# Kernel optimization log

Hardware: AMD Instinct MI355X
Metric: run time of the kernel (lower is better)

## Reference

```python
import jax, jax.numpy as jnp
import numpy as np

B, T, C = 2, 2048, 1024
H = 16
D = C // H          # 64
HID = C // 4        # meta_net bottleneck = 256
FF = 4 * C          # 4096


def setup_inputs() -> dict:
    key = jax.random.key(0)
    ks = jax.random.split(key, 11)
    s = lambda fan_in: 1.0 / np.sqrt(fan_in)
    inp = {
        "x": jax.random.normal(ks[0], (B, T, C), jnp.float32),
        # torch nn.Linear weights are [out, in]
        "Wq": jax.random.uniform(ks[1], (C, C), jnp.float32, -s(C), s(C)),
        "Wk": jax.random.uniform(ks[2], (C, C), jnp.float32, -s(C), s(C)),
        "Wv": jax.random.uniform(ks[3], (C, C), jnp.float32, -s(C), s(C)),
        "Wm1": jax.random.uniform(ks[4], (HID, C), jnp.float32, -s(C), s(C)),
        "bm1": jax.random.uniform(ks[5], (HID,), jnp.float32, -s(C), s(C)),
        "Wm2": jax.random.uniform(ks[6], (H, HID), jnp.float32, -s(HID), s(HID)),
        "bm2": jax.random.uniform(ks[7], (H,), jnp.float32, -s(HID), s(HID)),
        "Wproj": jax.random.uniform(ks[8], (C, C), jnp.float32, -s(C), s(C)),
        "Wfc": jax.random.uniform(ks[9], (FF, C), jnp.float32, -s(C), s(C)),
        "Wcp": jax.random.uniform(ks[10], (C, FF), jnp.float32, -s(FF), s(FF)),
    }
    return inp


def _rms_norm(x):
    eps = jnp.finfo(x.dtype).eps
    return x * jax.lax.rsqrt(jnp.mean(jnp.square(x), axis=-1, keepdims=True) + eps)


def reference(x, Wq, Wk, Wv, Wm1, bm1, Wm2, bm2, Wproj, Wfc, Wcp):
    b, t, c = x.shape
    h = Wm2.shape[0]
    d = c // h
    q = (x @ Wq.T).reshape(b, t, h, d)
    k = (x @ Wk.T).reshape(b, t, h, d)
    v = (x @ Wv.T).reshape(b, t, h, d)
    surprise = jax.nn.sigmoid(jnp.maximum(x @ Wm1.T + bm1, 0.0) @ Wm2.T + bm2)  # [b,t,h]
    decay = 1.0 - surprise

    # time-major for scan: [t, b, h, ...]
    qT = jnp.transpose(q, (1, 0, 2, 3))
    kT = jnp.transpose(k, (1, 0, 2, 3))
    vT = jnp.transpose(v, (1, 0, 2, 3))
    dT = jnp.transpose(decay, (1, 0, 2))     # [t,b,h]
    gT = jnp.transpose(surprise, (1, 0, 2))  # [t,b,h]

    def step(state, inp):
        qt, kt, vt, dt, gt = inp
        # state: [b,h,d,d]; decay-gated rank-1 update
        state = state * dt[..., None, None] + gt[..., None, None] * (kt[..., :, None] * vt[..., None, :])
        yt = jnp.einsum('bhd,bhde->bhe', qt, state)
        return state, yt

    state0 = jnp.zeros((b, h, d, d), x.dtype)
    _, ys = jax.lax.scan(step, state0, (qT, kT, vT, dT, gT))  # ys: [t,b,h,d]
    y = jnp.transpose(ys, (1, 0, 2, 3)).reshape(b, t, c)
    y = y @ Wproj.T
    yn = _rms_norm(y)
    mlp = jnp.square(jnp.maximum(yn @ Wfc.T, 0.0)) @ Wcp.T
    return y + mlp
```

## Files before the change

kernel.cpp:

```cpp
#include <hip/hip_runtime.h>
#include <math.h>

#define BB   2
#define TT   2048
#define CC   1024
#define HH   16
#define DD   64
#define HID  256
#define FFD  4096
#define NTOK (BB*TT)
#define CT   64
#define NC   (TT/CT)
#define NBH  (BB*HH)
#define NCHK (NBH*NC)
#define MB   (1048576ULL)

typedef unsigned short u16;
typedef unsigned int   u32;
typedef __attribute__((ext_vector_type(8))) short frag8;
typedef __attribute__((ext_vector_type(4))) float f32x4;

__device__ __forceinline__ float bf2f(u16 h){
    union { u32 u; float f; } c; c.u = ((u32)h) << 16; return c.f;
}
__device__ __forceinline__ u16 f2bf(float f){
    union { float f; u32 u; } c; c.f = f;
    u32 u = c.u;
    u += 0x7FFFu + ((u >> 16) & 1u);
    return (u16)(u >> 16);
}
__device__ __forceinline__ bool is_f32(const u32* flags, int idx) {
    if (idx == -2) return true;
    if (idx < 0)  return false;
    return flags[idx] != 0;
}

__device__ __forceinline__ void gload16(const void* g, void* l) {
    __builtin_amdgcn_global_load_lds(
        (const __attribute__((address_space(1))) u32*)g,
        (__attribute__((address_space(3))) u32*)l, 16, 0, 0);
}

template<int N> __device__ __forceinline__ void wait_vm() {
    if constexpr (N == 0)      asm volatile("s_waitcnt vmcnt(0)" ::: "memory");
    else if constexpr (N == 4) asm volatile("s_waitcnt vmcnt(4)" ::: "memory");
    else                       asm volatile("s_waitcnt vmcnt(6)" ::: "memory");
}
__device__ __forceinline__ void barrier_raw() {
    asm volatile("s_barrier" ::: "memory");
}

struct InPtrs { const void* p[11]; int n[11]; };

__global__ __launch_bounds__(64)
void sniff_kernel(InPtrs ip, u32* __restrict__ flags)
{
    int lane = threadIdx.x;
    u32 f0 = 0;
    for (int i = 0; i < 11; i++) {
        const u16* p = (const u16*)ip.p[i];
        int cap = ip.n[i] < 256 ? ip.n[i] : 256;
        bool ok = true;
        for (int j = lane; j < cap; j += 64) {
            u16 u = p[j];
            u32 e = (u >> 7) & 0xFFu;
            bool good = (u == 0u) || (u == 0x8000u) || (e >= 64u && e < 192u);
            ok = ok && good;
        }
        unsigned long long ball = __ballot(ok);
        u32 fl = (ball == ~0ull) ? 0u : 1u;
        if (ip.n[i] < 64) fl = f0;
        if (i == 0) f0 = fl;
        if (lane == 0) flags[i] = fl;
    }
}

struct ConvArgs {
    const void* src[6];
    u16* dst[6];
    int flag[6];
    int bstart[7];
    int nseg;
};

__global__ __launch_bounds__(256)
void conv_kernel(ConvArgs a, const u32* __restrict__ flags)
{
    int b = blockIdx.x;
    int s = 0;
    #pragma unroll
    for (int i = 1; i < 6; i++) if (i < a.nseg && b >= a.bstart[i]) s = i;
    size_t off = ((size_t)(b - a.bstart[s])) * 2048 + (size_t)threadIdx.x * 8;
    u16* d = a.dst[s] + off;
    if (flags[a.flag[s]] != 0) {
        const float* sp = (const float*)a.src[s] + off;
        float4 x0 = *(const float4*)sp;
        float4 x1 = *(const float4*)(sp + 4);
        u16 buf[8];
        buf[0]=f2bf(x0.x); buf[1]=f2bf(x0.y); buf[2]=f2bf(x0.z); buf[3]=f2bf(x0.w);
        buf[4]=f2bf(x1.x); buf[5]=f2bf(x1.y); buf[6]=f2bf(x1.z); buf[7]=f2bf(x1.w);
        *(uint4*)d = *(uint4*)buf;
    } else {
        *(uint4*)d = *(const uint4*)((const u16*)a.src[s] + off);
    }
}

__device__ __forceinline__ void xcd_map(int i, int NB, int gx, int& bm, int& bn)
{
    int per = NB >> 3;
    int iq  = (i & 7) * per + (i >> 3);
    bm = iq / gx;
    bn = iq % gx;
}

template<int MODE, int BM, int BN, int KS>
__global__ __launch_bounds__(256)
void gemm_nt(const u16* __restrict__ A, const u16* __restrict__ B,
             void* Cm, void* Cm2, const void* aux,
             int M, int N, int K, int lda, int ldb,
             const u32* __restrict__ flags, int oi)
{
    constexpr int MFR = BM / 32;
    constexpr int NFR = BN / 32;
    constexpr int BKE = KS * 32;
    const bool of32 = is_f32(flags, oi);
    __shared__ u16 As[2][KS][BM * 32];
    __shared__ u16 Bs[2][KS][BN * 32];
    const int tid = threadIdx.x;
    int bm, bn;
    xcd_map(blockIdx.x, gridDim.x, N / BN, bm, bn);
    const int z = blockIdx.y;
    const size_t koff = (size_t)z * K;

    const int wave = tid >> 6, lane = tid & 63;
    const int lm = lane & 15, quad = lane >> 4;
    const int wm = (wave >> 1) * (BM / 2), wn = (wave & 1) * (BN / 2);

    const int srow = lane >> 2;
    const int scol = (lane & 3) * 8;
    const int arow = (BM == 128) ? (wave*32 + srow) : (wave*16 + srow);
    const int brow = (BN == 128) ? (wave*32 + srow) : (wave*16 + srow);
    const u16* gA = A + (size_t)(bm*BM + arow)*lda + koff + scol;
    const u16* gB = B + (size_t)(bn*BN + brow)*ldb + koff + scol;
    const size_t a16 = (size_t)16 * lda, b16 = (size_t)16 * ldb;

    f32x4 acc[MFR][NFR];
    #pragma unroll
    for (int i = 0; i < MFR; i++)
        #pragma unroll
        for (int j = 0; j < NFR; j++)
            acc[i][j] = (f32x4){0.f, 0.f, 0.f, 0.f};

    auto stage = [&](int buf, int kk) {
        #pragma unroll
        for (int ks = 0; ks < KS; ks++) {
            if constexpr (BM == 128) {
                gload16(gA + kk + ks*32,       &As[buf][ks][wave*1024]);
                gload16(gA + kk + ks*32 + a16, &As[buf][ks][wave*1024 + 512]);
            } else {
                gload16(gA + kk + ks*32, &As[buf][ks][wave*512]);
            }
            if constexpr (BN == 128) {
                gload16(gB + kk + ks*32,       &Bs[buf][ks][wave*1024]);
                gload16(gB + kk + ks*32 + b16, &Bs[buf][ks][wave*1024 + 512]);
            } else {
                gload16(gB + kk + ks*32, &Bs[buf][ks][wave*512]);
            }
        }
    };

    stage(0, 0);
    __syncthreads();
    int cur = 0;
    for (int k0 = 0; k0 < K; k0 += BKE) {
        if (k0 + BKE < K) stage(cur ^ 1, k0 + BKE);
        #pragma unroll
        for (int ks = 0; ks < KS; ks++) {
            frag8 af[MFR], bfr[NFR];
            #pragma unroll
            for (int i = 0; i < MFR; i++)
                af[i]  = *(frag8*)&As[cur][ks][(wm + i*16 + lm)*32 + quad*8];
            #pragma unroll
            for (int j = 0; j < NFR; j++)
                bfr[j] = *(frag8*)&Bs[cur][ks][(wn + j*16 + lm)*32 + quad*8];
            #pragma unroll
            for (int i = 0; i < MFR; i++)
                #pragma unroll
                for (int j = 0; j < NFR; j++)
                    acc[i][j] = __builtin_amdgcn_mfma_f32_16x16x32_bf16(
                        af[i], bfr[j], acc[i][j], 0, 0, 0);
        }
        __syncthreads();
        cur ^= 1;
    }

    float* outF = (float*)(z ? Cm2 : Cm);
    #pragma unroll
    for (int i = 0; i < MFR; i++) {
        #pragma unroll
        for (int j = 0; j < NFR; j++) {
            const int gcol = bn*BN + wn + j*16 + lm;
            #pragma unroll
            for (int r = 0; r < 4; r++) {
                const int grow = bm*BM + wm + i*16 + quad*4 + r;
                size_t off = (size_t)grow * N + gcol;
                float vv = acc[i][j][r];
                if constexpr (MODE == 0) {
                    outF[off] = vv;
                } else if constexpr (MODE == 2) {
                    vv = fmaxf(vv, 0.f);
                    ((u16*)Cm)[off] = f2bf(vv * vv);
                } else {
                    float res = of32 ? ((const float*)aux)[off]
                                     : bf2f(((const u16*)aux)[off]);
                    vv += res;
                    if (of32) ((float*)Cm)[off] = vv;
                    else      ((u16*)Cm)[off]   = f2bf(vv);
                }
            }
        }
    }
}

__global__ __launch_bounds__(512)
void gemm_fc8(const u16* __restrict__ A, const u16* __restrict__ B,
              u16* __restrict__ C)
{
    __shared__ u16 As[2][256 * 64];
    __shared__ u16 Bs[2][256 * 64];
    const int tid = threadIdx.x;
    int bm, bn;
    xcd_map(blockIdx.x, 256, 16, bm, bn);

    const int w = tid >> 6, lane = tid & 63;
    const int lm = lane & 15, quad = lane >> 4;
    const int wm = (w >> 2) * 128, wn = (w & 3) * 64;

    const int srow = tid >> 3;
    const int scol = (((tid & 7) ^ ((tid >> 3) & 7))) * 8;
    const u16* gA = A + (size_t)(bm*256 + srow)*1024 + scol;
    const u16* gB = B + (size_t)(bn*256 + srow)*1024 + scol;

    auto stageA = [&](int buf, int h, int t1) {
        size_t ko = (size_t)t1 * 64;
        #pragma unroll
        for (int q = 0; q < 2; q++)
            gload16(gA + (size_t)(h*128 + q*64)*1024 + ko,
                    &As[buf][(h*128 + q*64 + w*8)*64]);
    };
    auto stageB = [&](int buf, int h, int t1) {
        size_t ko = (size_t)t1 * 64;
        #pragma unroll
        for (int q = 0; q < 2; q++)
            gload16(gB + (size_t)(h*128 + q*64)*1024 + ko,
                    &Bs[buf][(h*128 + q*64 + w*8)*64]);
    };

    f32x4 acc[8][4];
    #pragma unroll
    for (int i = 0; i < 8; i++)
        #pragma unroll
        for (int j = 0; j < 4; j++)
            acc[i][j] = (f32x4){0.f, 0.f, 0.f, 0.f};

    constexpr int NT = 16;
    stageA(0, 0, 0); stageB(0, 0, 0); stageA(0, 1, 0); stageB(0, 1, 0);

    const int rsw = (lm & 7);
    for (int t = 0; t < NT; ++t) {
        const int cur = t & 1;
        const bool more = (t + 1 < NT);
        #pragma unroll
        for (int p = 0; p < 4; ++p) {
            if (more) {
                if (p == 0)      stageA(cur ^ 1, 0, t + 1);
                else if (p == 1) stageB(cur ^ 1, 0, t + 1);
                else if (p == 2) stageA(cur ^ 1, 1, t + 1);
                else             stageB(cur ^ 1, 1, t + 1);
            }
            if (p == 0) { if (more) wait_vm<6>(); else wait_vm<4>(); }
            if (p == 1) { if (more) wait_vm<4>(); else wait_vm<0>(); }
            barrier_raw();
            const int rh = p >> 1, ch = p & 1;
            frag8 af[4][2], bfr[2][2];
            #pragma unroll
            for (int i = 0; i < 4; i++)
                #pragma unroll
                for (int kk = 0; kk < 2; kk++)
                    af[i][kk] = *(frag8*)&As[cur][(wm + rh*64 + i*16 + lm)*64
                                      + (((kk*4 + quad) ^ rsw) * 8)];
            #pragma unroll
            for (int j = 0; j < 2; j++)
                #pragma unroll
                for (int kk = 0; kk < 2; kk++)
                    bfr[j][kk] = *(frag8*)&Bs[cur][(wn + ch*32 + j*16 + lm)*64
                                      + (((kk*4 + quad) ^ rsw) * 8)];
            __builtin_amdgcn_s_setprio(1);
            #pragma unroll
            for (int kk = 0; kk < 2; kk++)
                #pragma unroll
                for (int i = 0; i < 4; i++)
                    #pragma unroll
                    for (int j = 0; j < 2; j++)
                        acc[rh*4 + i][ch*2 + j] =
                            __builtin_amdgcn_mfma_f32_16x16x32_bf16(
                                af[i][kk], bfr[j][kk], acc[rh*4 + i][ch*2 + j],
                                0, 0, 0);
            __builtin_amdgcn_s_setprio(0);
        }
    }

    #pragma unroll
    for (int I = 0; I < 8; I++) {
        #pragma unroll
        for (int J = 0; J < 4; J++) {
            const int gcol = bn*256 + wn + (J >> 1)*32 + (J & 1)*16 + lm;
            #pragma unroll
            for (int r = 0; r < 4; r++) {
                const int grow = bm*256 + wm + (I >> 2)*64 + (I & 3)*16
                               + quad*4 + r;
                float vv = fmaxf(acc[I][J][r], 0.f);
                C[(size_t)grow * FFD + gcol] = f2bf(vv * vv);
            }
        }
    }
}

__global__ __launch_bounds__(256)
void gemm_qkvm(const u16* __restrict__ xb,
               const u16* __restrict__ Wqb, const u16* __restrict__ Wkb,
               const u16* __restrict__ Wvb, const u16* __restrict__ Wm1b,
               const void* __restrict__ bm1,
               u16* __restrict__ q, u16* __restrict__ k, u16* __restrict__ v,
               float* __restrict__ hid, const u32* __restrict__ flags)
{
    __shared__ u16 As[2][128 * 32];
    __shared__ u16 Bs[2][128 * 32];
    const int tid = threadIdx.x;
    int bm, bn;
    xcd_map(blockIdx.x, 832, 26, bm, bn);

    const int bsel = bn >> 3;
    const u16* B = (bsel == 0) ? Wqb : (bsel == 1) ? Wkb
                 : (bsel == 2) ? Wvb : Wm1b;

    const int wave = tid >> 6, lane = tid & 63;
    const int lm = lane & 15, quad = lane >> 4;
    const int wm = (wave >> 1) * 64, wn = (wave & 1) * 64;

    const int srow = lane >> 2;
    const int scol = (lane & 3) * 8;
    const u16* gA = xb + (size_t)(bm*128 + wave*32 + srow)*CC + scol;
    const u16* gB = B + (size_t)((bn & 7)*128 + wave*32 + srow)*CC + scol;
    const size_t s16 = (size_t)16 * CC;

    f32x4 acc[4][4];
    #pragma unroll
    for (int i = 0; i < 4; i++)
        #pragma unroll
        for (int j = 0; j < 4; j++)
            acc[i][j] = (f32x4){0.f, 0.f, 0.f, 0.f};

    auto stage = [&](int buf, int kk) {
        gload16(gA + kk,       &As[buf][wave*1024]);
        gload16(gA + kk + s16, &As[buf][wave*1024 + 512]);
        gload16(gB + kk,       &Bs[buf][wave*1024]);
        gload16(gB + kk + s16, &Bs[buf][wave*1024 + 512]);
    };

    stage(0, 0);
    __syncthreads();
    int cur = 0;
    for (int k0 = 0; k0 < CC; k0 += 32) {
        if (k0 + 32 < CC) stage(cur ^ 1, k0 + 32);
        frag8 af[4], bfr[4];
        #pragma unroll
        for (int i = 0; i < 4; i++) {
            af[i]  = *(frag8*)&As[cur][(wm + i*16 + lm)*32 + quad*8];
            bfr[i] = *(frag8*)&Bs[cur][(wn + i*16 + lm)*32 + quad*8];
        }
        #pragma unroll
        for (int i = 0; i < 4; i++)
            #pragma unroll
            for (int j = 0; j < 4; j++)
                acc[i][j] = __builtin_amdgcn_mfma_f32_16x16x32_bf16(
                    af[i], bfr[j], acc[i][j], 0, 0, 0);
        __syncthreads();
        cur ^= 1;
    }

    if (bsel < 3) {
        u16* outp = (bsel == 0) ? q : (bsel == 1) ? k : v;
        #pragma unroll
        for (int i = 0; i < 4; i++) {
            #pragma unroll
            for (int j = 0; j < 4; j++) {
                const int gcol = (bn & 7)*128 + wn + j*16 + lm;
                #pragma unroll
                for (int r = 0; r < 4; r++) {
                    const int grow = bm*128 + wm + i*16 + quad*4 + r;
                    outp[(size_t)grow * CC + gcol] = f2bf(acc[i][j][r]);
                }
            }
        }
    } else {
        const bool biasf = is_f32(flags, 5);
        #pragma unroll
        for (int i = 0; i < 4; i++) {
            #pragma unroll
            for (int j = 0; j < 4; j++) {
                const int gcol = (bn & 7)*128 + wn + j*16 + lm;
                float bia = biasf ? ((const float*)bm1)[gcol]
                                  : bf2f(((const u16*)bm1)[gcol]);
                #pragma unroll
                for (int r = 0; r < 4; r++) {
                    const int grow = bm*128 + wm + i*16 + quad*4 + r;
                    hid[(size_t)grow * HID + gcol] = fmaxf(acc[i][j][r] + bia, 0.f);
                }
            }
        }
    }
}

__global__ __launch_bounds__(256)
void meta2_kernel(const float* __restrict__ hid, const void* __restrict__ Wm2,
                  const void* __restrict__ bm2, float* __restrict__ g,
                  float* __restrict__ dec, const u32* __restrict__ flags)
{
    const bool wf = is_f32(flags, 6);
    const bool bf = is_f32(flags, 7);
    __shared__ float hs[16][257];
    __shared__ float wsm[16][257];
    int tid  = threadIdx.x;
    int tok0 = blockIdx.x * 16;
    for (int i = tid; i < 16*256; i += 256) {
        wsm[i >> 8][i & 255] = wf ? ((const float*)Wm2)[i] : bf2f(((const u16*)Wm2)[i]);
        hs [i >> 8][i & 255] = hid[(size_t)tok0*256 + i];
    }
    __syncthreads();
    int tok = tid >> 4, hh = tid & 15;
    float s = 0.f;
    #pragma unroll 8
    for (int kk = 0; kk < 256; kk++) s = fmaf(hs[tok][kk], wsm[hh][kk], s);
    s += bf ? ((const float*)bm2)[hh] : bf2f(((const u16*)bm2)[hh]);
    float sg = 1.f / (1.f + expf(-s));
    int idx = (tok0 + tok) * HH + hh;
    g[idx]   = sg;
    dec[idx] = 1.f - sg;
}

__device__ __forceinline__ void cum_prefix(const float* dd, float* cum, int tid)
{
    if (tid < 64) {
        float lw = logf(fmaxf(dd[tid], 1e-30f));
        #pragma unroll
        for (int off = 1; off < 64; off <<= 1) {
            float nv = __shfl_up(lw, off, 64);
            if (tid >= off) lw += nv;
        }
        cum[tid] = lw;
    }
    __syncthreads();
}

__global__ __launch_bounds__(256)
void scan_pass1(const u16* __restrict__ kbuf, const u16* __restrict__ vbuf,
                const float* __restrict__ g, const float* __restrict__ dec,
                float* __restrict__ Mb, float* __restrict__ Pb)
{
    __shared__ u16 kt[64*72];
    __shared__ u16 vt[64*72];
    __shared__ float dd[64], gg[64], cum[64], sw[64];
    int tid = threadIdx.x;
    int bhc = blockIdx.x;
    int c = bhc & 31, h = (bhc >> 5) & 15, b = bhc >> 9;
    int t0 = c * CT;
    size_t rowbase = ((size_t)(b*TT + t0))*CC + h*DD;

    if (tid < 64) {
        int gidx = (b*TT + t0 + tid)*HH + h;
        dd[tid] = dec[gidx];
        gg[tid] = g[gidx];
    }
    __syncthreads();
    cum_prefix(dd, cum, tid);
    float ctot = cum[63];
    if (tid < 64) sw[tid] = gg[tid] * expf(ctot - cum[tid]);
    __syncthreads();

    #pragma unroll 4
    for (int i = tid; i < 4096; i += 256) {
        int ss = i >> 6, d = i & 63;
        size_t gi = rowbase + (size_t)ss*CC + d;
        kt[d*72 + ss] = f2bf(sw[ss] * bf2f(kbuf[gi]));
        vt[d*72 + ss] = vbuf[gi];
    }
    __syncthreads();

    const int w = tid >> 6, lane = tid & 63;
    const int lm = lane & 15, quad = lane >> 4;

    f32x4 mf[4];
    #pragma unroll
    for (int j = 0; j < 4; j++) mf[j] = (f32x4){0.f,0.f,0.f,0.f};
    #pragma unroll
    for (int kk = 0; kk < 2; kk++) {
        frag8 aK = *(frag8*)&kt[(w*16 + lm)*72 + kk*32 + quad*8];
        #pragma unroll
        for (int j = 0; j < 4; j++) {
            frag8 bV = *(frag8*)&vt[(j*16 + lm)*72 + kk*32 + quad*8];
            mf[j] = __builtin_amdgcn_mfma_f32_16x16x32_bf16(aK, bV, mf[j], 0, 0, 0);
        }
    }

    size_t base = (size_t)bhc * 4096;
    #pragma unroll
    for (int r = 0; r < 4; r++) {
        int d = w*16 + quad*4 + r;
        #pragma unroll
        for (int j = 0; j < 4; j++)
            Mb[base + (size_t)d*64 + j*16 + lm] = mf[j][r];
    }
    if (tid == 0) Pb[bhc] = expf(ctot);
}

__global__ __launch_bounds__(256)
void scan_pass2(float* __restrict__ MS, const float* __restrict__ Pb)
{
    int bh = blockIdx.x >> 4, grp = blockIdx.x & 15, tid = threadIdx.x;
    int eo = grp*256 + tid;
    float st = 0.f;
    for (int c = 0; c < NC; c++) {
        size_t e = ((size_t)bh*NC + c) * 4096 + eo;
        float p = Pb[bh*NC + c];
        float m = MS[e];
        MS[e] = st;
        st = fmaf(p, st, m);
    }
}

__global__ __launch_bounds__(256)
void scan_pass3(const u16* __restrict__ qbuf, const u16* __restrict__ kbuf,
                const u16* __restrict__ vbuf, const float* __restrict__ g,
                const float* __restrict__ dec, const float* __restrict__ Sb,
                u16* __restrict__ y)
{
    __shared__ u16 qs16[64*72];
    __shared__ u16 ks16[64*72];
    __shared__ u16 vt16[64*72];
    __shared__ u16 aws16[64*72];
    __shared__ float Ss_t[64*68];
    __shared__ float dd[64], gg[64], cum[64];
    int tid = threadIdx.x;
    int bhc = blockIdx.x;
    int c = bhc & 31, h = (bhc >> 5) & 15, b = bhc >> 9;
    int t0 = c * CT;
    size_t rowbase = ((size_t)(b*TT + t0))*CC + h*DD;
    size_t sbase = (size_t)bhc * 4096;

    {
        int sr = tid >> 2, d0 = (tid & 3) * 16;
        size_t gq = rowbase + (size_t)sr*CC + d0;
        *(uint4*)&qs16[sr*72 + d0]     = *(const uint4*)&qbuf[gq];
        *(uint4*)&qs16[sr*72 + d0 + 8] = *(const uint4*)&qbuf[gq + 8];
        *(uint4*)&ks16[sr*72 + d0]     = *(const uint4*)&kbuf[gq];
        *(uint4*)&ks16[sr*72 + d0 + 8] = *(const uint4*)&kbuf[gq + 8];
        #pragma unroll 4
        for (int i = tid; i < 4096; i += 256) {
            int ss = i >> 6, e = i & 63;
            vt16[e*72 + ss] = vbuf[rowbase + (size_t)ss*CC + e];
        }
        int dr = tid >> 2, e0 = (tid & 3) * 16;
        #pragma unroll
        for (int m = 0; m < 4; m++) {
            float4 sv4 = *(const float4*)&Sb[sbase + (size_t)dr*64 + e0 + m*4];
            Ss_t[(e0 + m*4 + 0)*68 + dr] = sv4.x;
            Ss_t[(e0 + m*4 + 1)*68 + dr] = sv4.y;
            Ss_t[(e0 + m*4 + 2)*68 + dr] = sv4.z;
            Ss_t[(e0 + m*4 + 3)*68 + dr] = sv4.w;
        }
        if (tid < 64) {
            int gidx = (b*TT + t0 + tid)*HH + h;
            dd[tid] = dec[gidx];
            gg[tid] = g[gidx];
        }
    }
    __syncthreads();
    cum_prefix(dd, cum, tid);

    const int w = tid >> 6, lane = tid & 63;
    const int lm = lane & 15, quad = lane >> 4;

    f32x4 a1f[4];
    #pragma unroll
    for (int j = 0; j < 4; j++) a1f[j] = (f32x4){0.f,0.f,0.f,0.f};
    #pragma unroll
    for (int kk = 0; kk < 2; kk++) {
        frag8 aq = *(frag8*)&qs16[(w*16 + lm)*72 + kk*32 + quad*8];
        #pragma unroll
        for (int j = 0; j < 4; j++) {
            frag8 bk = *(frag8*)&ks16[(j*16 + lm)*72 + kk*32 + quad*8];
            a1f[j] = __builtin_amdgcn_mfma_f32_16x16x32_bf16(aq, bk, a1f[j], 0, 0, 0);
        }
    }

    #pragma unroll
    for (int j = 0; j < 4; j++) {
        #pragma unroll
        for (int r = 0; r < 4; r++) {
            int t = w*16 + quad*4 + r, s = j*16 + lm;
            float wgt = (s <= t) ? gg[s] * expf(cum[t] - cum[s]) : 0.f;
            aws16[t*72 + s] = f2bf(wgt * a1f[j][r]);
        }
    }
    __syncthreads();

    f32x4 of[4];
    #pragma unroll
    for (int j = 0; j < 4; j++) of[j] = (f32x4){0.f,0.f,0.f,0.f};
    #pragma unroll
    for (int kk = 0; kk < 2; kk++) {
        frag8 aA = *(frag8*)&aws16[(w*16 + lm)*72 + kk*32 + quad*8];
        #pragma unroll
        for (int j = 0; j < 4; j++) {
            frag8 bV = *(frag8*)&vt16[(j*16 + lm)*72 + kk*32 + quad*8];
            of[j] = __builtin_amdgcn_mfma_f32_16x16x32_bf16(aA, bV, of[j], 0, 0, 0);
        }
    }

    float o2v[4][4] = {};
    for (int d8 = 0; d8 < 8; d8++) {
        frag8 qr[4];
        #pragma unroll
        for (int r = 0; r < 4; r++)
            qr[r] = *(frag8*)&qs16[(w*16 + quad*4 + r)*72 + d8*8];
        float qv[4][8];
        #pragma unroll
        for (int r = 0; r < 4; r++)
            #pragma unroll
            for (int d2 = 0; d2 < 8; d2++)
                qv[r][d2] = bf2f((u16)qr[r][d2]);
        #pragma unroll
        for (int j = 0; j < 4; j++) {
            int e = j*16 + lm;
            float4 s0 = *(float4*)&Ss_t[e*68 + d8*8];
            float4 s1 = *(float4*)&Ss_t[e*68 + d8*8 + 4];
            float sv[8] = {s0.x, s0.y, s0.z, s0.w, s1.x, s1.y, s1.z, s1.w};
            #pragma unroll
            for (int d2 = 0; d2 < 8; d2++)
                #pragma unroll
                for (int r = 0; r < 4; r++)
                    o2v[j][r] = fmaf(qv[r][d2], sv[d2], o2v[j][r]);
        }
    }

    #pragma unroll
    for (int r = 0; r < 4; r++) {
        int t = w*16 + quad*4 + r;
        float cd = expf(cum[t]);
        size_t obase = rowbase + (size_t)t*CC;
        #pragma unroll
        for (int j = 0; j < 4; j++)
            y[obase + j*16 + lm] = f2bf(fmaf(cd, o2v[j][r], of[j][r]));
    }
}

__global__ __launch_bounds__(256)
void rmsnorm_kernel(const float* __restrict__ p0, const float* __restrict__ p1,
                    void* __restrict__ yres, u16* __restrict__ yn,
                    const u32* __restrict__ flags)
{
    const bool of32 = flags[0] != 0;
    __shared__ float red[4];
    __shared__ float sscale;
    int row = blockIdx.x, tid = threadIdx.x;
    size_t base = (size_t)row*CC + tid*4;
    float4 a = *(const float4*)&p0[base];
    float4 b = *(const float4*)&p1[base];
    float v0 = a.x + b.x, v1 = a.y + b.y, v2 = a.z + b.z, v3 = a.w + b.w;
    if (of32) {
        *(float4*)((float*)yres + base) = make_float4(v0, v1, v2, v3);
    } else {
        u16* yr = (u16*)yres + base;
        yr[0] = f2bf(v0); yr[1] = f2bf(v1); yr[2] = f2bf(v2); yr[3] = f2bf(v3);
    }
    float p = v0*v0 + v1*v1 + v2*v2 + v3*v3;
    #pragma unroll
    for (int off = 32; off > 0; off >>= 1) p += __shfl_down(p, off, 64);
    if ((tid & 63) == 0) red[tid >> 6] = p;
    __syncthreads();
    if (tid == 0) {
        float tot = red[0] + red[1] + red[2] + red[3];
        sscale = rsqrtf(tot * (1.0f/1024.0f) + 1.1920928955078125e-07f);
    }
    __syncthreads();
    float sc = sscale;
    yn[base + 0] = f2bf(v0 * sc);
    yn[base + 1] = f2bf(v1 * sc);
    yn[base + 2] = f2bf(v2 * sc);
    yn[base + 3] = f2bf(v3 * sc);
}

extern "C" void kernel_launch(void* const* d_in, const int* in_sizes, int n_in,
                              void* d_out, int out_size, void* d_ws, size_t ws_size,
                              hipStream_t stream)
{
    char* ws = (char*)d_ws;
    u16*   xb     = (u16*)  (ws + 32*MB);
    u16*   Wqb    = (u16*)  (ws + 40*MB);
    u16*   Wkb    = (u16*)  (ws + 42*MB);
    u16*   Wvb    = (u16*)  (ws + 44*MB);
    u16*   Wm1b   = (u16*)  (ws + 46*MB);
    u16*   Wprojb = (u16*)  (ws + 8*MB);
    u16*   q      = (u16*)  (ws + 0*MB);
    u16*   k      = (u16*)  (ws + 16*MB);
    u16*   v      = (u16*)  (ws + 24*MB);
    float* hid    = (float*)(ws + 10*MB);
    float* g      = (float*)(ws + 14*MB);
    float* dec    = (float*)(ws + 14*MB + 262144);
    float* Pb     = (float*)(ws + 14*MB + 524288);
    float* MS     = (float*)(ws + 32*MB);
    u16*   yat    = q;
    float* p0     = (float*)(ws + 16*MB);
    float* p1     = (float*)(ws + 32*MB);
    u16*   yn     = (u16*)  (ws + 0*MB);
    u16*   Wfcb   = (u16*)  (ws + 8*MB);
    u16*   h1     = (u16*)  (ws + 16*MB);
    u16*   Wcpb   = (u16*)  (ws + 0*MB);
    u32*   flags  = (u32*)  (ws + 48*MB);

    InPtrs ip;
    for (int i = 0; i < 11; i++) { ip.p[i] = d_in[i]; ip.n[i] = in_sizes[i]; }
    sniff_kernel<<<1, 64, 0, stream>>>(ip, flags);

    ConvArgs c1{};
    c1.src[0] = d_in[0]; c1.dst[0] = xb;     c1.flag[0] = 0;
    c1.src[1] = d_in[1]; c1.dst[1] = Wqb;    c1.flag[1] = 1;
    c1.src[2] = d_in[2]; c1.dst[2] = Wkb;    c1.flag[2] = 2;
    c1.src[3] = d_in[3]; c1.dst[3] = Wvb;    c1.flag[3] = 3;
    c1.src[4] = d_in[4]; c1.dst[4] = Wm1b;   c1.flag[4] = 4;
    c1.src[5] = d_in[8]; c1.dst[5] = Wprojb; c1.flag[5] = 8;
    {
        int nb[6] = {2048, 512, 512, 512, 128, 512};
        int cum = 0;
        for (int i = 0; i < 6; i++) { c1.bstart[i] = cum; cum += nb[i]; }
        c1.bstart[6] = cum;
        c1.nseg = 6;
        conv_kernel<<<cum, 256, 0, stream>>>(c1, flags);
    }

    gemm_qkvm<<<832, 256, 0, stream>>>(xb, Wqb, Wkb, Wvb, Wm1b, d_in[5],
                                       q, k, v, hid, flags);
    meta2_kernel<<<NTOK/16, 256, 0, stream>>>(hid, d_in[6], d_in[7], g, dec, flags);
    scan_pass1<<<NCHK, 256, 0, stream>>>(k, v, g, dec, MS, Pb);
    scan_pass2<<<NBH*16, 256, 0, stream>>>(MS, Pb);
    scan_pass3<<<NCHK, 256, 0, stream>>>(q, k, v, g, dec, MS, yat);
    gemm_nt<0,128,128,1><<<dim3(256, 2), 256, 0, stream>>>(yat, Wprojb, p0, p1,
        nullptr, NTOK, CC, 512, CC, CC, flags, -2);
    ConvArgs c2{};
    c2.src[0] = d_in[9]; c2.dst[0] = Wfcb; c2.flag[0] = 9;
    c2.bstart[0] = 0; for (int i = 1; i < 7; i++) c2.bstart[i] = 2048;
    c2.nseg = 1;
    conv_kernel<<<2048, 256, 0, stream>>>(c2, flags);
    rmsnorm_kernel<<<NTOK, 256, 0, stream>>>(p0, p1, d_out, yn, flags);
    gemm_fc8<<<256, 512, 0, stream>>>(yn, Wfcb, h1);
    ConvArgs c3{};
    c3.src[0] = d_in[10]; c3.dst[0] = Wcpb; c3.flag[0] = 10;
    c3.bstart[0] = 0; for (int i = 1; i < 7; i++) c3.bstart[i] = 2048;
    c3.nseg = 1;
    conv_kernel<<<2048, 256, 0, stream>>>(c3, flags);
    gemm_nt<3,64,64,2><<<dim3(1024, 1), 256, 0, stream>>>(h1, Wcpb, d_out, nullptr,
        d_out, NTOK, CC, FFD, FFD, FFD, flags, 0);
}
```

Baseline: 368.6 us.

## Rewrite QKV/meta GEMM as 256x256-tile, 8-wave kernel with swizzled LDS pipeline

Replaces the 128x128-tile, 4-wave QKV+meta1 GEMM with a 256x256-tile, 512-thread kernel using BK=64, XOR-swizzled LDS layout and a staged double-buffer pipeline with fine-grained vmcnt waits and raw barriers. The launch drops from 832 blocks to 208. The larger tiles raise operand reuse per block and the swizzle avoids LDS bank conflicts. Fewer blocks (208 on a GPU with many CUs) risks underfilling the device, and the large LDS footprint limits occupancy.

```diff
diff --git a/kernel.cpp b/kernel.cpp
--- a/kernel.cpp
+++ b/kernel.cpp
@@ -326,96 +326,133 @@
     }
 }
 
-__global__ __launch_bounds__(256)
-void gemm_qkvm(const u16* __restrict__ xb,
-               const u16* __restrict__ Wqb, const u16* __restrict__ Wkb,
-               const u16* __restrict__ Wvb, const u16* __restrict__ Wm1b,
-               const void* __restrict__ bm1,
-               u16* __restrict__ q, u16* __restrict__ k, u16* __restrict__ v,
-               float* __restrict__ hid, const u32* __restrict__ flags)
-{
-    __shared__ u16 As[2][128 * 32];
-    __shared__ u16 Bs[2][128 * 32];
+__global__ __launch_bounds__(512)
+void gemm_qkvm8(const u16* __restrict__ xb,
+                const u16* __restrict__ Wqb, const u16* __restrict__ Wkb,
+                const u16* __restrict__ Wvb, const u16* __restrict__ Wm1b,
+                const void* __restrict__ bm1,
+                u16* __restrict__ q, u16* __restrict__ k, u16* __restrict__ v,
+                float* __restrict__ hid, const u32* __restrict__ flags)
+{
+    __shared__ u16 As[2][256 * 64];
+    __shared__ u16 Bs[2][256 * 64];
     const int tid = threadIdx.x;
     int bm, bn;
-    xcd_map(blockIdx.x, 832, 26, bm, bn);
-
-    const int bsel = bn >> 3;
-    const u16* B = (bsel == 0) ? Wqb : (bsel == 1) ? Wkb
-                 : (bsel == 2) ? Wvb : Wm1b;
-
-    const int wave = tid >> 6, lane = tid & 63;
+    xcd_map(blockIdx.x, 208, 13, bm, bn);
+
+    const int bsel = (bn < 12) ? (bn >> 2) : 3;
+    const int bcol = (bn < 12) ? (bn & 3) * 256 : 0;
+    const u16* Bp = (bsel == 0) ? Wqb : (bsel == 1) ? Wkb
+                  : (bsel == 2) ? Wvb : Wm1b;
+
+    const int w = tid >> 6, lane = tid & 63;
     const int lm = lane & 15, quad = lane >> 4;
-    const int wm = (wave >> 1) * 64, wn = (wave & 1) * 64;
-
-    const int srow = lane >> 2;
-    const int scol = (lane & 3) * 8;
-    const u16* gA = xb + (size_t)(bm*128 + wave*32 + srow)*CC + scol;
-    const u16* gB = B + (size_t)((bn & 7)*128 + wave*32 + srow)*CC + scol;
-    const size_t s16 = (size_t)16 * CC;
-
-    f32x4 acc[4][4];
-    #pragma unroll
-    for (int i = 0; i < 4; i++)
+    const int wm = (w >> 2) * 128, wn = (w & 3) * 64;
+
+    const int srow = tid >> 3;
+    const int scol = (((tid & 7) ^ ((tid >> 3) & 7))) * 8;
+    const u16* gA = xb + (size_t)(bm*256 + srow)*1024 + scol;
+    const u16* gB = Bp + (size_t)(bcol + srow)*1024 + scol;
+
+    auto stageA = [&](int buf, int h, int t1) {
+        size_t ko = (size_t)t1 * 64;
+        #pragma unroll
+        for (int qq = 0; qq < 2; qq++)
+            gload16(gA + (size_t)(h*128 + qq*64)*1024 + ko,
+                    &As[buf][(h*128 + qq*64 + w*8)*64]);
+    };
+    auto stageB = [&](int buf, int h, int t1) {
+        size_t ko = (size_t)t1 * 64;
+        #pragma unroll
+        for (int qq = 0; qq < 2; qq++)
+            gload16(gB + (size_t)(h*128 + qq*64)*1024 + ko,
+                    &Bs[buf][(h*128 + qq*64 + w*8)*64]);
+    };
+
+    f32x4 acc[8][4];
+    #pragma unroll
+    for (int i = 0; i < 8; i++)
         #pragma unroll
         for (int j = 0; j < 4; j++)
             acc[i][j] = (f32x4){0.f, 0.f, 0.f, 0.f};
 
-    auto stage = [&](int buf, int kk) {
-        gload16(gA + kk,       &As[buf][wave*1024]);
-        gload16(gA + kk + s16, &As[buf][wave*1024 + 512]);
-        gload16(gB + kk,       &Bs[buf][wave*1024]);
-        gload16(gB + kk + s16, &Bs[buf][wave*1024 + 512]);
-    };
-
-    stage(0, 0);
-    __syncthreads();
-    int cur = 0;
-    for (int k0 = 0; k0 < CC; k0 += 32) {
-        if (k0 + 32 < CC) stage(cur ^ 1, k0 + 32);
-        frag8 af[4], bfr[4];
-        #pragma unroll
-        for (int i = 0; i < 4; i++) {
-            af[i]  = *(frag8*)&As[cur][(wm + i*16 + lm)*32 + quad*8];
-            bfr[i] = *(frag8*)&Bs[cur][(wn + i*16 + lm)*32 + quad*8];
-        }
-        #pragma unroll
-        for (int i = 0; i < 4; i++)
-            #pragma unroll
-            for (int j = 0; j < 4; j++)
-                acc[i][j] = __builtin_amdgcn_mfma_f32_16x16x32_bf16(
-                    af[i], bfr[j], acc[i][j], 0, 0, 0);
-        __syncthreads();
-        cur ^= 1;
+    constexpr int NT = 16;
+    stageA(0, 0, 0); stageB(0, 0, 0); stageA(0, 1, 0); stageB(0, 1, 0);
+
+    const int rsw = (lm & 7);
+    for (int t = 0; t < NT; ++t) {
+        const int cur = t & 1;
+        const bool more = (t + 1 < NT);
+        #pragma unroll
+        for (int p = 0; p < 4; ++p) {
+            if (more) {
+                if (p == 0)      stageA(cur ^ 1, 0, t + 1);
+                else if (p == 1) stageB(cur ^ 1, 0, t + 1);
+                else if (p == 2) stageA(cur ^ 1, 1, t + 1);
+                else             stageB(cur ^ 1, 1, t + 1);
+            }
+            if (p == 0) { if (more) wait_vm<6>(); else wait_vm<4>(); }
+            if (p == 1) { if (more) wait_vm<4>(); else wait_vm<0>(); }
+            barrier_raw();
+            const int rh = p >> 1, ch = p & 1;
+            frag8 af[4][2], bfr[2][2];
+            #pragma unroll
+            for (int i = 0; i < 4; i++)
+                #pragma unroll
+                for (int kk = 0; kk < 2; kk++)
+                    af[i][kk] = *(frag8*)&As[cur][(wm + rh*64 + i*16 + lm)*64
+                                      + (((kk*4 + quad) ^ rsw) * 8)];
+            #pragma unroll
+            for (int j = 0; j < 2; j++)
+                #pragma unroll
+                for (int kk = 0; kk < 2; kk++)
+                    bfr[j][kk] = *(frag8*)&Bs[cur][(wn + ch*32 + j*16 + lm)*64
+                                      + (((kk*4 + quad) ^ rsw) * 8)];
+            __builtin_amdgcn_s_setprio(1);
+            #pragma unroll
+            for (int kk = 0; kk < 2; kk++)
+                #pragma unroll
+                for (int i = 0; i < 4; i++)
+                    #pragma unroll
+                    for (int j = 0; j < 2; j++)
+                        acc[rh*4 + i][ch*2 + j] =
+                            __builtin_amdgcn_mfma_f32_16x16x32_bf16(
+                                af[i][kk], bfr[j][kk], acc[rh*4 + i][ch*2 + j],
+                                0, 0, 0);
+            __builtin_amdgcn_s_setprio(0);
+        }
     }
 
     if (bsel < 3) {
         u16* outp = (bsel == 0) ? q : (bsel == 1) ? k : v;
         #pragma unroll
-        for (int i = 0; i < 4; i++) {
-            #pragma unroll
-            for (int j = 0; j < 4; j++) {
-                const int gcol = (bn & 7)*128 + wn + j*16 + lm;
+        for (int I = 0; I < 8; I++) {
+            #pragma unroll
+            for (int J = 0; J < 4; J++) {
+                const int gcol = bcol + wn + (J >> 1)*32 + (J & 1)*16 + lm;
                 #pragma unroll
                 for (int r = 0; r < 4; r++) {
-                    const int grow = bm*128 + wm + i*16 + quad*4 + r;
-                    outp[(size_t)grow * CC + gcol] = f2bf(acc[i][j][r]);
+                    const int grow = bm*256 + wm + (I >> 2)*64 + (I & 3)*16
+                                   + quad*4 + r;
+                    outp[(size_t)grow * CC + gcol] = f2bf(acc[I][J][r]);
                 }
             }
         }
     } else {
         const bool biasf = is_f32(flags, 5);
         #pragma unroll
-        for (int i = 0; i < 4; i++) {
-            #pragma unroll
-            for (int j = 0; j < 4; j++) {
-                const int gcol = (bn & 7)*128 + wn + j*16 + lm;
+        for (int I = 0; I < 8; I++) {
+            #pragma unroll
+            for (int J = 0; J < 4; J++) {
+                const int gcol = wn + (J >> 1)*32 + (J & 1)*16 + lm;
                 float bia = biasf ? ((const float*)bm1)[gcol]
                                   : bf2f(((const u16*)bm1)[gcol]);
                 #pragma unroll
                 for (int r = 0; r < 4; r++) {
-                    const int grow = bm*128 + wm + i*16 + quad*4 + r;
-                    hid[(size_t)grow * HID + gcol] = fmaxf(acc[i][j][r] + bia, 0.f);
+                    const int grow = bm*256 + wm + (I >> 2)*64 + (I & 3)*16
+                                   + quad*4 + r;
+                    hid[(size_t)grow * HID + gcol] =
+                        fmaxf(acc[I][J][r] + bia, 0.f);
                 }
             }
         }
@@ -749,8 +786,8 @@
         conv_kernel<<<cum, 256, 0, stream>>>(c1, flags);
     }
 
-    gemm_qkvm<<<832, 256, 0, stream>>>(xb, Wqb, Wkb, Wvb, Wm1b, d_in[5],
-                                       q, k, v, hid, flags);
+    gemm_qkvm8<<<208, 512, 0, stream>>>(xb, Wqb, Wkb, Wvb, Wm1b, d_in[5],
+                                        q, k, v, hid, flags);
     meta2_kernel<<<NTOK/16, 256, 0, stream>>>(hid, d_in[6], d_in[7], g, dec, flags);
     scan_pass1<<<NCHK, 256, 0, stream>>>(k, v, g, dec, MS, Pb);
     scan_pass2<<<NBH*16, 256, 0, stream>>>(MS, Pb);
```

Result: faster. 359.8 us (-2.4%).
